# Optimization experiments

Hardware: AMD Instinct MI355X
Metric: run time of the kernel (lower is better)

The kernel has to match this reference:

```python
import jax, jax.numpy as jnp
import numpy as np

D_MODEL = 1024
N_HEADS = 16
D_K = D_MODEL // N_HEADS
D_FF = 4096
B, S = 4, 2048
EPS = 1e-5


def setup_inputs() -> dict:
    key = jax.random.key(0)
    ks = jax.random.split(key, 16)
    s = 0.02
    inp = {
        'x': jax.random.normal(ks[0], (B, S, D_MODEL), dtype=jnp.float32),
        'Wq': jax.random.normal(ks[1], (D_MODEL, D_MODEL), dtype=jnp.float32) * s,
        'bq': jnp.zeros((D_MODEL,), jnp.float32),
        'Wk': jax.random.normal(ks[2], (D_MODEL, D_MODEL), dtype=jnp.float32) * s,
        'bk': jnp.zeros((D_MODEL,), jnp.float32),
        'Wv': jax.random.normal(ks[3], (D_MODEL, D_MODEL), dtype=jnp.float32) * s,
        'bv': jnp.zeros((D_MODEL,), jnp.float32),
        'Wo': jax.random.normal(ks[4], (D_MODEL, D_MODEL), dtype=jnp.float32) * s,
        'bo': jnp.zeros((D_MODEL,), jnp.float32),
        'W1': jax.random.normal(ks[5], (D_MODEL, D_FF), dtype=jnp.float32) * s,
        'b1': jnp.zeros((D_FF,), jnp.float32),
        'W2': jax.random.normal(ks[6], (D_FF, D_MODEL), dtype=jnp.float32) * s,
        'b2': jnp.zeros((D_MODEL,), jnp.float32),
        'g1': jnp.ones((D_MODEL,), jnp.float32),
        'be1': jnp.zeros((D_MODEL,), jnp.float32),
        'g2': jnp.ones((D_MODEL,), jnp.float32),
        'be2': jnp.zeros((D_MODEL,), jnp.float32),
    }
    return inp


def _layernorm(x, g, b):
    mu = jnp.mean(x, axis=-1, keepdims=True)
    var = jnp.var(x, axis=-1, keepdims=True)
    return (x - mu) * jax.lax.rsqrt(var + EPS) * g + b


def reference(x, Wq, bq, Wk, bk, Wv, bv, Wo, bo, W1, b1, W2, b2, g1, be1, g2, be2):
    # Multi-head self-attention (mask=None, dropout in eval -> identity)
    q = (x @ Wq + bq).reshape(B, S, N_HEADS, D_K).transpose(0, 2, 1, 3)  # [B,H,S,Dk]
    k = (x @ Wk + bk).reshape(B, S, N_HEADS, D_K).transpose(0, 2, 1, 3)
    v = (x @ Wv + bv).reshape(B, S, N_HEADS, D_K).transpose(0, 2, 1, 3)
    scores = jnp.einsum('bhqd,bhkd->bhqk', q, k) / jnp.sqrt(jnp.float32(D_K))
    attn = jax.nn.softmax(scores, axis=-1)
    out = jnp.einsum('bhqk,bhkd->bhqd', attn, v)          # [B,H,S,Dk]
    out = out.transpose(0, 2, 1, 3).reshape(B, S, D_MODEL)
    att_out = out @ Wo + bo
    x2 = _layernorm(x + att_out, g1, be1)
    ff = jax.nn.relu(x2 @ W1 + b1) @ W2 + b2
    return _layernorm(x2 + ff, g2, be2)
```

## Files before the change

kernel.cpp:

```cpp
#include <hip/hip_runtime.h>
#include <hip/hip_bf16.h>

typedef __attribute__((ext_vector_type(8)))  __bf16 bf16x8;
typedef __attribute__((ext_vector_type(4)))  float  f32x4;
typedef __attribute__((ext_vector_type(16))) float  f32x16;

static __device__ __forceinline__ unsigned short f2bf(float x) {
    unsigned int u = __float_as_uint(x);
    unsigned int r = (u + 0x7FFFu + ((u >> 16) & 1u)) >> 16;
    return (unsigned short)r;
}

static __device__ __forceinline__ float fast_exp2(float x) {
    float r;
    asm volatile("v_exp_f32 %0, %1\n\ts_nop 1" : "=v"(r) : "v"(x));
    return r;
}
static __device__ __forceinline__ unsigned int cvt_pk_bf16(float a, float b) {
    unsigned int r;
    asm("v_cvt_pk_bf16_f32 %0, %1, %2" : "=v"(r) : "v"(a), "v"(b));
    return r;
}

static __device__ __forceinline__ void gload_lds16(const ushort* g, ushort* l) {
    __builtin_amdgcn_global_load_lds((const __attribute__((address_space(1))) void*)g,
                                     (__attribute__((address_space(3))) void*)l, 16, 0, 0);
}

static __device__ __forceinline__ int xcd_swz(int id, int nwg) {
    return (id & 7) * (nwg >> 3) + (id >> 3);
}

__global__ __launch_bounds__(256) void cast_bf16_kernel(const float* __restrict__ in,
                                                        ushort* __restrict__ out, int n4) {
    int i = blockIdx.x * 256 + threadIdx.x;
    if (i < n4) {
        float4 v = reinterpret_cast<const float4*>(in)[i];
        ushort4 o;
        o.x = f2bf(v.x); o.y = f2bf(v.y); o.z = f2bf(v.z); o.w = f2bf(v.w);
        reinterpret_cast<ushort4*>(out)[i] = o;
    }
}

__global__ __launch_bounds__(256) void transpose_cast_kernel(const float* __restrict__ in,
                                                             ushort* __restrict__ out,
                                                             int K, int N) {
    __shared__ float tile[32][33];
    const int tx = threadIdx.x;
    const int ty = threadIdx.y;
    const int n0 = blockIdx.x * 32;
    const int k0 = blockIdx.y * 32;
    for (int i = ty; i < 32; i += 8)
        tile[i][tx] = in[(size_t)(k0 + i) * N + n0 + tx];
    __syncthreads();
    for (int i = ty; i < 32; i += 8)
        out[(size_t)(n0 + i) * K + k0 + tx] = f2bf(tile[tx][i]);
}

template<int RELU, int OUTBF>
__global__ __launch_bounds__(256) void gemm_bt(const ushort* __restrict__ A,
                                               const ushort* __restrict__ Bt,
                                               const float* __restrict__ bias,
                                               void* __restrict__ Cp,
                                               int M, int N, int K) {
    __shared__ ushort As[128 * 32];
    __shared__ ushort Bs[128 * 32];
    const int tid  = threadIdx.x;
    const int lane = tid & 63;
    const int w    = tid >> 6;
    const int wr   = w >> 1, wc = w & 1;
    const int nwg = gridDim.x * gridDim.y;
    int wid = xcd_swz(blockIdx.y * gridDim.x + blockIdx.x, nwg);
    const int bx = wid % gridDim.x;
    const int by = wid / gridDim.x;
    const int m0 = by * 128;
    const int n0 = bx * 128;
    const int lr = lane & 15;
    const int lk = (lane >> 4) * 8;

    const int r0 = w * 32 + (lane >> 2);
    const int c8 = (lane & 3) * 8;
    const ushort* gA0 = A  + (size_t)(m0 + r0)      * K + c8;
    const ushort* gA1 = A  + (size_t)(m0 + r0 + 16) * K + c8;
    const ushort* gB0 = Bt + (size_t)(n0 + r0)      * K + c8;
    const ushort* gB1 = Bt + (size_t)(n0 + r0 + 16) * K + c8;
    ushort* lA0 = &As[w * 1024];
    ushort* lA1 = &As[w * 1024 + 512];
    ushort* lB0 = &Bs[w * 1024];
    ushort* lB1 = &Bs[w * 1024 + 512];

    f32x4 acc[4][4];
    const f32x4 z = {0.f, 0.f, 0.f, 0.f};
    for (int i = 0; i < 4; i++) for (int j = 0; j < 4; j++) acc[i][j] = z;

    for (int k0 = 0; k0 < K; k0 += 32) {
        __syncthreads();
        gload_lds16(gA0 + k0, lA0);
        gload_lds16(gA1 + k0, lA1);
        gload_lds16(gB0 + k0, lB0);
        gload_lds16(gB1 + k0, lB1);
        __syncthreads();

        bf16x8 af[4], bfr[4];
        for (int i = 0; i < 4; i++)
            af[i] = *reinterpret_cast<const bf16x8*>(&As[(wr * 64 + i * 16 + lr) * 32 + lk]);
        for (int j = 0; j < 4; j++)
            bfr[j] = *reinterpret_cast<const bf16x8*>(&Bs[(wc * 64 + j * 16 + lr) * 32 + lk]);
        for (int i = 0; i < 4; i++)
            for (int j = 0; j < 4; j++)
                acc[i][j] = __builtin_amdgcn_mfma_f32_16x16x32_bf16(af[i], bfr[j], acc[i][j], 0, 0, 0);
    }

    const int rbase = (lane >> 4) * 4;
    for (int i = 0; i < 4; i++) {
        for (int j = 0; j < 4; j++) {
            const int col = n0 + wc * 64 + j * 16 + lr;
            const float bv = bias[col];
            for (int r = 0; r < 4; r++) {
                const int row = m0 + wr * 64 + i * 16 + rbase + r;
                float v = acc[i][j][r] + bv;
                if (RELU) v = v > 0.f ? v : 0.f;
                if (OUTBF) ((ushort*)Cp)[(size_t)row * N + col] = f2bf(v);
                else       ((float*)Cp)[(size_t)row * N + col] = v;
            }
        }
    }
}

__global__ __launch_bounds__(256) void gemm_qkv(const ushort* __restrict__ A,
                                                const ushort* __restrict__ Bt,
                                                const float* __restrict__ bq,
                                                const float* __restrict__ bk,
                                                const float* __restrict__ bv,
                                                ushort* __restrict__ Cp) {
    const int K = 1024, N = 3072;
    __shared__ ushort As[128 * 32];
    __shared__ ushort Bs[128 * 32];
    const int tid  = threadIdx.x;
    const int lane = tid & 63;
    const int w    = tid >> 6;
    const int wr   = w >> 1, wc = w & 1;
    const int nwg = gridDim.x * gridDim.y;
    int wid = xcd_swz(blockIdx.y * gridDim.x + blockIdx.x, nwg);
    const int bx = wid % gridDim.x;
    const int by = wid / gridDim.x;
    const int m0 = by * 128;
    const int n0 = bx * 128;
    const int lr = lane & 15;
    const int lk = (lane >> 4) * 8;

    const int r0 = w * 32 + (lane >> 2);
    const int c8 = (lane & 3) * 8;
    const ushort* gA0 = A  + (size_t)(m0 + r0)      * K + c8;
    const ushort* gA1 = A  + (size_t)(m0 + r0 + 16) * K + c8;
    const ushort* gB0 = Bt + (size_t)(n0 + r0)      * K + c8;
    const ushort* gB1 = Bt + (size_t)(n0 + r0 + 16) * K + c8;
    ushort* lA0 = &As[w * 1024];
    ushort* lA1 = &As[w * 1024 + 512];
    ushort* lB0 = &Bs[w * 1024];
    ushort* lB1 = &Bs[w * 1024 + 512];

    f32x4 acc[4][4];
    const f32x4 z = {0.f, 0.f, 0.f, 0.f};
    for (int i = 0; i < 4; i++) for (int j = 0; j < 4; j++) acc[i][j] = z;

    for (int k0 = 0; k0 < K; k0 += 32) {
        __syncthreads();
        gload_lds16(gA0 + k0, lA0);
        gload_lds16(gA1 + k0, lA1);
        gload_lds16(gB0 + k0, lB0);
        gload_lds16(gB1 + k0, lB1);
        __syncthreads();

        bf16x8 af[4], bfr[4];
        for (int i = 0; i < 4; i++)
            af[i] = *reinterpret_cast<const bf16x8*>(&As[(wr * 64 + i * 16 + lr) * 32 + lk]);
        for (int j = 0; j < 4; j++)
            bfr[j] = *reinterpret_cast<const bf16x8*>(&Bs[(wc * 64 + j * 16 + lr) * 32 + lk]);
        for (int i = 0; i < 4; i++)
            for (int j = 0; j < 4; j++)
                acc[i][j] = __builtin_amdgcn_mfma_f32_16x16x32_bf16(af[i], bfr[j], acc[i][j], 0, 0, 0);
    }

    const float* bias = (n0 < 1024) ? bq : (n0 < 2048 ? bk : bv);
    const float qscale = (n0 < 1024) ? 0.18033688f : 1.0f;
    const int nb = n0 & 1023;
    const int rbase = (lane >> 4) * 4;
    for (int i = 0; i < 4; i++) {
        for (int j = 0; j < 4; j++) {
            const int cloc = wc * 64 + j * 16 + lr;
            const float bv_ = bias[nb + cloc];
            for (int r = 0; r < 4; r++) {
                const int row = m0 + wr * 64 + i * 16 + rbase + r;
                Cp[(size_t)row * 3072 + n0 + cloc] = f2bf((acc[i][j][r] + bv_) * qscale);
            }
        }
    }
}

#define ASWZ(row, col) ((row) * 64 + ((col) ^ ((((row) ^ ((row) >> 3)) & 7) << 3)))

__global__ __launch_bounds__(256, 3) void attn_kernel(const ushort* __restrict__ QKV,
                                                      ushort* __restrict__ O) {
    __shared__ ushort Ks[2][4096];
    __shared__ ushort Vt[2][4096];
    __shared__ ushort Ps[4][2048];
    const int tid  = threadIdx.x;
    const int lane = tid & 63;
    const int w    = tid >> 6;
    const int l31  = lane & 31;
    const int hi   = lane >> 5;

    int blk = xcd_swz(blockIdx.x, gridDim.x);
    const int qb = blk & 15;
    const int h  = (blk >> 4) & 15;
    const int b  = blk >> 8;
    const int s0 = qb * 128 + w * 32;
    const size_t rowb   = (size_t)b * 2048;
    const size_t base_q = rowb * 3072 + (size_t)h * 64;
    const size_t base_k = base_q + 1024;
    const size_t base_v = base_q + 2048;
    const size_t base_o = rowb * 1024 + (size_t)h * 64;

    bf16x8 qf[4];
#pragma unroll
    for (int ks = 0; ks < 4; ks++)
        qf[ks] = *reinterpret_cast<const bf16x8*>(
            &QKV[base_q + (size_t)(s0 + l31) * 3072 + ks * 16 + 8 * hi]);

    int off8[2][4];
#pragma unroll
    for (int sub = 0; sub < 2; sub++)
#pragma unroll
        for (int ks = 0; ks < 4; ks++)
            off8[sub][ks] = ASWZ(sub * 32 + l31, ks * 16 + 8 * hi);
    int psoff[2][4][2];
#pragma unroll
    for (int ts = 0; ts < 2; ts++)
#pragma unroll
        for (int q4 = 0; q4 < 4; q4++)
#pragma unroll
            for (int e = 0; e < 2; e++)
                psoff[ts][q4][e] = ASWZ(l31, ts * 32 + 8 * q4 + 4 * hi + 2 * e);

    const int tS  = tid >> 3;
    const int ccS = tid & 7;
    int vwoff[2][8];
#pragma unroll
    for (int i = 0; i < 2; i++)
#pragma unroll
        for (int jj = 0; jj < 8; jj++)
            vwoff[i][jj] = ASWZ(ccS * 8 + jj, tS + i * 32);
    const int t1  = tS + 32;
    const int sz0 = (tS ^ (tS >> 3)) & 7;
    const int sz1 = (t1 ^ (t1 >> 3)) & 7;
    const ushort* pK0 = QKV + base_k + (size_t)tS * 3072 + (ccS ^ sz0) * 8;
    const ushort* pK1 = QKV + base_k + (size_t)t1 * 3072 + (ccS ^ sz1) * 8;
    const ushort* pV0 = QKV + base_v + (size_t)tS * 3072 + ccS * 8;
    const ushort* pV1 = QKV + base_v + (size_t)t1 * 3072 + ccS * 8;
    const size_t step = (size_t)64 * 3072;
    ushort* psw = Ps[w];

    gload_lds16(pK0, &Ks[0][w * 512]);
    gload_lds16(pK1, &Ks[0][2048 + w * 512]);
    {
        int4 v0 = *reinterpret_cast<const int4*>(pV0);
        int4 v1 = *reinterpret_cast<const int4*>(pV1);
        const ushort* vs0 = reinterpret_cast<const ushort*>(&v0);
        const ushort* vs1 = reinterpret_cast<const ushort*>(&v1);
#pragma unroll
        for (int jj = 0; jj < 8; jj++) Vt[0][vwoff[0][jj]] = vs0[jj];
#pragma unroll
        for (int jj = 0; jj < 8; jj++) Vt[0][vwoff[1][jj]] = vs1[jj];
    }
    pK0 += step; pK1 += step; pV0 += step; pV1 += step;
    __syncthreads();

    f32x16 oacc0 = {0.f}, oacc1 = {0.f};
    for (int i = 0; i < 16; i++) { oacc0[i] = 0.f; oacc1[i] = 0.f; }
    float lacc = 0.f;
    int cur = 0;

    for (int it = 0; it < 32; ++it) {
        int4 nv0, nv1;
        if (it < 31) {
            gload_lds16(pK0, &Ks[cur ^ 1][w * 512]);
            gload_lds16(pK1, &Ks[cur ^ 1][2048 + w * 512]);
            nv0 = *reinterpret_cast<const int4*>(pV0);
            nv1 = *reinterpret_cast<const int4*>(pV1);
            pK0 += step; pK1 += step; pV0 += step; pV1 += step;
        }

        f32x16 sa0 = {0.f}, sa1 = {0.f};
        for (int i = 0; i < 16; i++) { sa0[i] = 0.f; sa1[i] = 0.f; }
        __builtin_amdgcn_s_setprio(1);
#pragma unroll
        for (int ks = 0; ks < 4; ks++) {
            bf16x8 k0 = *reinterpret_cast<const bf16x8*>(&Ks[cur][off8[0][ks]]);
            sa0 = __builtin_amdgcn_mfma_f32_32x32x16_bf16(k0, qf[ks], sa0, 0, 0, 0);
        }
#pragma unroll
        for (int ks = 0; ks < 4; ks++) {
            bf16x8 k1 = *reinterpret_cast<const bf16x8*>(&Ks[cur][off8[1][ks]]);
            sa1 = __builtin_amdgcn_mfma_f32_32x32x16_bf16(k1, qf[ks], sa1, 0, 0, 0);
        }
        __builtin_amdgcn_s_setprio(0);

#pragma unroll
        for (int q4 = 0; q4 < 4; q4++)
#pragma unroll
            for (int e = 0; e < 2; e++) {
                float plo = fast_exp2(sa0[4 * q4 + 2 * e]);
                float phi = fast_exp2(sa0[4 * q4 + 2 * e + 1]);
                lacc += plo + phi;
                *reinterpret_cast<unsigned int*>(&psw[psoff[0][q4][e]]) = cvt_pk_bf16(plo, phi);
            }
#pragma unroll
        for (int q4 = 0; q4 < 4; q4++)
#pragma unroll
            for (int e = 0; e < 2; e++) {
                float plo = fast_exp2(sa1[4 * q4 + 2 * e]);
                float phi = fast_exp2(sa1[4 * q4 + 2 * e + 1]);
                lacc += plo + phi;
                *reinterpret_cast<unsigned int*>(&psw[psoff[1][q4][e]]) = cvt_pk_bf16(plo, phi);
            }

        __builtin_amdgcn_s_setprio(1);
#pragma unroll
        for (int ks = 0; ks < 4; ks++) {
            bf16x8 pa = *reinterpret_cast<const bf16x8*>(&psw[off8[0][ks]]);
            bf16x8 v0 = *reinterpret_cast<const bf16x8*>(&Vt[cur][off8[0][ks]]);
            oacc0 = __builtin_amdgcn_mfma_f32_32x32x16_bf16(pa, v0, oacc0, 0, 0, 0);
            bf16x8 v1 = *reinterpret_cast<const bf16x8*>(&Vt[cur][off8[1][ks]]);
            oacc1 = __builtin_amdgcn_mfma_f32_32x32x16_bf16(pa, v1, oacc1, 0, 0, 0);
        }
        __builtin_amdgcn_s_setprio(0);

        if (it < 31) {
            const ushort* vs0 = reinterpret_cast<const ushort*>(&nv0);
            const ushort* vs1 = reinterpret_cast<const ushort*>(&nv1);
#pragma unroll
            for (int jj = 0; jj < 8; jj++) Vt[cur ^ 1][vwoff[0][jj]] = vs0[jj];
#pragma unroll
            for (int jj = 0; jj < 8; jj++) Vt[cur ^ 1][vwoff[1][jj]] = vs1[jj];
        }
        __syncthreads();
        cur ^= 1;
    }

    const float ltot = lacc + __shfl_xor(lacc, 32);
    const float inv  = 1.f / ltot;

#pragma unroll
    for (int r = 0; r < 16; r++) {
        const int qloc = (r & 3) + 8 * (r >> 2) + 4 * hi;
        const float invq = __shfl(inv, qloc);
        const size_t rowoff = base_o + (size_t)(s0 + qloc) * 1024 + l31;
        O[rowoff]      = f2bf(oacc0[r] * invq);
        O[rowoff + 32] = f2bf(oacc1[r] * invq);
    }
}

__global__ __launch_bounds__(256) void ln_res_kernel(const float* __restrict__ x,
                                                     const float* __restrict__ y,
                                                     const float* __restrict__ g,
                                                     const float* __restrict__ be,
                                                     float* __restrict__ outf,
                                                     ushort* __restrict__ outb) {
    const int row = blockIdx.x;
    const int tid = threadIdx.x;
    const float4 xv = reinterpret_cast<const float4*>(x + (size_t)row * 1024)[tid];
    const float4 yv = reinterpret_cast<const float4*>(y + (size_t)row * 1024)[tid];
    float v[4] = {xv.x + yv.x, xv.y + yv.y, xv.z + yv.z, xv.w + yv.w};
    float s  = v[0] + v[1] + v[2] + v[3];
    float s2 = v[0]*v[0] + v[1]*v[1] + v[2]*v[2] + v[3]*v[3];
    for (int off = 32; off; off >>= 1) { s += __shfl_down(s, off); s2 += __shfl_down(s2, off); }
    __shared__ float red[8];
    const int w = tid >> 6, lane = tid & 63;
    if (lane == 0) { red[w] = s; red[4 + w] = s2; }
    __syncthreads();
    if (tid == 0) {
        const float ts  = red[0] + red[1] + red[2] + red[3];
        const float ts2 = red[4] + red[5] + red[6] + red[7];
        const float mu  = ts * (1.f / 1024.f);
        const float var = ts2 * (1.f / 1024.f) - mu * mu;
        red[0] = mu;
        red[1] = rsqrtf(var + 1e-5f);
    }
    __syncthreads();
    const float mu = red[0], rs = red[1];
    float4 of;
    ushort4 ob;
    const float4 gv = reinterpret_cast<const float4*>(g)[tid];
    const float4 bv = reinterpret_cast<const float4*>(be)[tid];
    of.x = (v[0] - mu) * rs * gv.x + bv.x;
    of.y = (v[1] - mu) * rs * gv.y + bv.y;
    of.z = (v[2] - mu) * rs * gv.z + bv.z;
    of.w = (v[3] - mu) * rs * gv.w + bv.w;
    reinterpret_cast<float4*>(outf + (size_t)row * 1024)[tid] = of;
    if (outb) {
        ob.x = f2bf(of.x); ob.y = f2bf(of.y); ob.z = f2bf(of.z); ob.w = f2bf(of.w);
        reinterpret_cast<ushort4*>(outb + (size_t)row * 1024)[tid] = ob;
    }
}

extern "C" void kernel_launch(void* const* d_in, const int* in_sizes, int n_in,
                              void* d_out, int out_size, void* d_ws, size_t ws_size,
                              hipStream_t stream) {
    const float* x  = (const float*)d_in[0];
    const float* Wq = (const float*)d_in[1];  const float* bq = (const float*)d_in[2];
    const float* Wk = (const float*)d_in[3];  const float* bk = (const float*)d_in[4];
    const float* Wv = (const float*)d_in[5];  const float* bv = (const float*)d_in[6];
    const float* Wo = (const float*)d_in[7];  const float* bo = (const float*)d_in[8];
    const float* W1 = (const float*)d_in[9];  const float* b1 = (const float*)d_in[10];
    const float* W2 = (const float*)d_in[11]; const float* b2 = (const float*)d_in[12];
    const float* g1 = (const float*)d_in[13]; const float* be1 = (const float*)d_in[14];
    const float* g2 = (const float*)d_in[15]; const float* be2 = (const float*)d_in[16];

    char* ws = (char*)d_ws;
    const size_t MBy = (size_t)1 << 20;
    ushort* xb    = (ushort*)(ws + 0 * MBy);
    ushort* wqkvT = (ushort*)(ws + 16 * MBy);
    ushort* woT   = (ushort*)(ws + 22 * MBy);
    ushort* w1T   = (ushort*)(ws + 24 * MBy);
    ushort* w2T   = (ushort*)(ws + 32 * MBy);
    ushort* QKVb  = (ushort*)(ws + 40 * MBy);
    ushort* AOb   = (ushort*)(ws + 88 * MBy);
    ushort* h1    = (ushort*)(ws + 40 * MBy);
    float*  y1    = (float*)(ws + 104 * MBy);
    float*  y2    = (float*)(ws + 104 * MBy);
    float*  x2f   = (float*)(ws + 136 * MBy);
    ushort* x2b   = (ushort*)(ws + 168 * MBy);
    (void)ws_size; (void)n_in; (void)in_sizes; (void)out_size;

    const int M = 8192;

    cast_bf16_kernel<<<(M * 1024 / 4 + 255) / 256, 256, 0, stream>>>(x, xb, M * 1024 / 4);
    dim3 tb(32, 8);
    transpose_cast_kernel<<<dim3(32, 32),  tb, 0, stream>>>(Wq, wqkvT,               1024, 1024);
    transpose_cast_kernel<<<dim3(32, 32),  tb, 0, stream>>>(Wk, wqkvT + 1024 * 1024, 1024, 1024);
    transpose_cast_kernel<<<dim3(32, 32),  tb, 0, stream>>>(Wv, wqkvT + 2048 * 1024, 1024, 1024);
    transpose_cast_kernel<<<dim3(32, 32),  tb, 0, stream>>>(Wo, woT, 1024, 1024);
    transpose_cast_kernel<<<dim3(128, 32), tb, 0, stream>>>(W1, w1T, 1024, 4096);
    transpose_cast_kernel<<<dim3(32, 128), tb, 0, stream>>>(W2, w2T, 4096, 1024);

    gemm_qkv<<<dim3(24, 64), 256, 0, stream>>>(xb, wqkvT, bq, bk, bv, QKVb);

    attn_kernel<<<1024, 256, 0, stream>>>(QKVb, AOb);

    gemm_bt<0, 0><<<dim3(8, 64), 256, 0, stream>>>(AOb, woT, bo, y1, M, 1024, 1024);

    ln_res_kernel<<<M, 256, 0, stream>>>(x, y1, g1, be1, x2f, x2b);

    gemm_bt<1, 1><<<dim3(32, 64), 256, 0, stream>>>(x2b, w1T, b1, h1, M, 4096, 1024);
    gemm_bt<0, 0><<<dim3(8, 64), 256, 0, stream>>>(h1, w2T, b2, y2, M, 1024, 4096);

    ln_res_kernel<<<M, 256, 0, stream>>>(x2f, y2, g2, be2, (float*)d_out, nullptr);
}
```

Before: 469.5 us.

## Keep P in registers via permlane swap; store intermediates as bf16

In the attention kernel the softmax probabilities were written to a per-wave LDS buffer and read back as the MFMA A operand. They are now packed in registers, and v_permlane32_swap rearranges them into operand layout, which removes that LDS traffic and frees its shared memory. Separately, the Wo and W2 GEMM outputs, and the residual x2 fed into the second layernorm, are stored as bf16 instead of fp32. This cuts global memory traffic in the GEMM epilogues and layernorm kernels. The cost is lower precision on the residual and pre-norm sums.

```diff
diff --git a/kernel.cpp b/kernel.cpp
--- a/kernel.cpp
+++ b/kernel.cpp
@@ -9,6 +9,9 @@
     unsigned int u = __float_as_uint(x);
     unsigned int r = (u + 0x7FFFu + ((u >> 16) & 1u)) >> 16;
     return (unsigned short)r;
+}
+static __device__ __forceinline__ float bf2f(unsigned short u) {
+    return __uint_as_float(((unsigned int)u) << 16);
 }
 
 static __device__ __forceinline__ float fast_exp2(float x) {
@@ -133,7 +136,7 @@
                                                 const float* __restrict__ bk,
                                                 const float* __restrict__ bv,
                                                 ushort* __restrict__ Cp) {
-    const int K = 1024, N = 3072;
+    const int K = 1024;
     __shared__ ushort As[128 * 32];
     __shared__ ushort Bs[128 * 32];
     const int tid  = threadIdx.x;
@@ -204,7 +207,6 @@
                                                       ushort* __restrict__ O) {
     __shared__ ushort Ks[2][4096];
     __shared__ ushort Vt[2][4096];
-    __shared__ ushort Ps[4][2048];
     const int tid  = threadIdx.x;
     const int lane = tid & 63;
     const int w    = tid >> 6;
@@ -234,14 +236,6 @@
 #pragma unroll
         for (int ks = 0; ks < 4; ks++)
             off8[sub][ks] = ASWZ(sub * 32 + l31, ks * 16 + 8 * hi);
-    int psoff[2][4][2];
-#pragma unroll
-    for (int ts = 0; ts < 2; ts++)
-#pragma unroll
-        for (int q4 = 0; q4 < 4; q4++)
-#pragma unroll
-            for (int e = 0; e < 2; e++)
-                psoff[ts][q4][e] = ASWZ(l31, ts * 32 + 8 * q4 + 4 * hi + 2 * e);
 
     const int tS  = tid >> 3;
     const int ccS = tid & 7;
@@ -259,7 +253,6 @@
     const ushort* pV0 = QKV + base_v + (size_t)tS * 3072 + ccS * 8;
     const ushort* pV1 = QKV + base_v + (size_t)t1 * 3072 + ccS * 8;
     const size_t step = (size_t)64 * 3072;
-    ushort* psw = Ps[w];
 
     gload_lds16(pK0, &Ks[0][w * 512]);
     gload_lds16(pK1, &Ks[0][2048 + w * 512]);
@@ -276,7 +269,7 @@
     pK0 += step; pK1 += step; pV0 += step; pV1 += step;
     __syncthreads();
 
-    f32x16 oacc0 = {0.f}, oacc1 = {0.f};
+    f32x16 oacc0, oacc1;
     for (int i = 0; i < 16; i++) { oacc0[i] = 0.f; oacc1[i] = 0.f; }
     float lacc = 0.f;
     int cur = 0;
@@ -291,7 +284,7 @@
             pK0 += step; pK1 += step; pV0 += step; pV1 += step;
         }
 
-        f32x16 sa0 = {0.f}, sa1 = {0.f};
+        f32x16 sa0, sa1;
         for (int i = 0; i < 16; i++) { sa0[i] = 0.f; sa1[i] = 0.f; }
         __builtin_amdgcn_s_setprio(1);
 #pragma unroll
@@ -306,33 +299,37 @@
         }
         __builtin_amdgcn_s_setprio(0);
 
-#pragma unroll
-        for (int q4 = 0; q4 < 4; q4++)
-#pragma unroll
-            for (int e = 0; e < 2; e++) {
-                float plo = fast_exp2(sa0[4 * q4 + 2 * e]);
-                float phi = fast_exp2(sa0[4 * q4 + 2 * e + 1]);
-                lacc += plo + phi;
-                *reinterpret_cast<unsigned int*>(&psw[psoff[0][q4][e]]) = cvt_pk_bf16(plo, phi);
-            }
-#pragma unroll
-        for (int q4 = 0; q4 < 4; q4++)
-#pragma unroll
-            for (int e = 0; e < 2; e++) {
-                float plo = fast_exp2(sa1[4 * q4 + 2 * e]);
-                float phi = fast_exp2(sa1[4 * q4 + 2 * e + 1]);
-                lacc += plo + phi;
-                *reinterpret_cast<unsigned int*>(&psw[psoff[1][q4][e]]) = cvt_pk_bf16(plo, phi);
-            }
+        unsigned pk0[8], pk1[8];
+#pragma unroll
+        for (int i = 0; i < 8; i++) {
+            float plo = fast_exp2(sa0[2 * i]);
+            float phi = fast_exp2(sa0[2 * i + 1]);
+            lacc += plo + phi;
+            pk0[i] = cvt_pk_bf16(plo, phi);
+        }
+#pragma unroll
+        for (int i = 0; i < 8; i++) {
+            float plo = fast_exp2(sa1[2 * i]);
+            float phi = fast_exp2(sa1[2 * i + 1]);
+            lacc += plo + phi;
+            pk1[i] = cvt_pk_bf16(plo, phi);
+        }
 
         __builtin_amdgcn_s_setprio(1);
 #pragma unroll
         for (int ks = 0; ks < 4; ks++) {
-            bf16x8 pa = *reinterpret_cast<const bf16x8*>(&psw[off8[0][ks]]);
+            const int bi = 4 * (ks & 1);
+            unsigned a, bb, c, d;
+            if (ks < 2) { a = pk0[bi]; bb = pk0[bi + 1]; c = pk0[bi + 2]; d = pk0[bi + 3]; }
+            else        { a = pk1[bi]; bb = pk1[bi + 1]; c = pk1[bi + 2]; d = pk1[bi + 3]; }
+            asm("v_permlane32_swap_b32 %0, %1" : "+v"(a), "+v"(c));
+            asm("v_permlane32_swap_b32 %0, %1" : "+v"(bb), "+v"(d));
+            union { unsigned u[4]; bf16x8 v; } fr;
+            fr.u[0] = a; fr.u[1] = bb; fr.u[2] = c; fr.u[3] = d;
             bf16x8 v0 = *reinterpret_cast<const bf16x8*>(&Vt[cur][off8[0][ks]]);
-            oacc0 = __builtin_amdgcn_mfma_f32_32x32x16_bf16(pa, v0, oacc0, 0, 0, 0);
+            oacc0 = __builtin_amdgcn_mfma_f32_32x32x16_bf16(fr.v, v0, oacc0, 0, 0, 0);
             bf16x8 v1 = *reinterpret_cast<const bf16x8*>(&Vt[cur][off8[1][ks]]);
-            oacc1 = __builtin_amdgcn_mfma_f32_32x32x16_bf16(pa, v1, oacc1, 0, 0, 0);
+            oacc1 = __builtin_amdgcn_mfma_f32_32x32x16_bf16(fr.v, v1, oacc1, 0, 0, 0);
         }
         __builtin_amdgcn_s_setprio(0);
 
@@ -361,17 +358,16 @@
     }
 }
 
-__global__ __launch_bounds__(256) void ln_res_kernel(const float* __restrict__ x,
-                                                     const float* __restrict__ y,
-                                                     const float* __restrict__ g,
-                                                     const float* __restrict__ be,
-                                                     float* __restrict__ outf,
-                                                     ushort* __restrict__ outb) {
+__global__ __launch_bounds__(256) void ln_res_fb(const float* __restrict__ x,
+                                                 const ushort* __restrict__ y,
+                                                 const float* __restrict__ g,
+                                                 const float* __restrict__ be,
+                                                 ushort* __restrict__ outb) {
     const int row = blockIdx.x;
     const int tid = threadIdx.x;
     const float4 xv = reinterpret_cast<const float4*>(x + (size_t)row * 1024)[tid];
-    const float4 yv = reinterpret_cast<const float4*>(y + (size_t)row * 1024)[tid];
-    float v[4] = {xv.x + yv.x, xv.y + yv.y, xv.z + yv.z, xv.w + yv.w};
+    const ushort4 yv = reinterpret_cast<const ushort4*>(y + (size_t)row * 1024)[tid];
+    float v[4] = {xv.x + bf2f(yv.x), xv.y + bf2f(yv.y), xv.z + bf2f(yv.z), xv.w + bf2f(yv.w)};
     float s  = v[0] + v[1] + v[2] + v[3];
     float s2 = v[0]*v[0] + v[1]*v[1] + v[2]*v[2] + v[3]*v[3];
     for (int off = 32; off; off >>= 1) { s += __shfl_down(s, off); s2 += __shfl_down(s2, off); }
@@ -389,19 +385,52 @@
     }
     __syncthreads();
     const float mu = red[0], rs = red[1];
-    float4 of;
-    ushort4 ob;
     const float4 gv = reinterpret_cast<const float4*>(g)[tid];
     const float4 bv = reinterpret_cast<const float4*>(be)[tid];
+    ushort4 ob;
+    ob.x = f2bf((v[0] - mu) * rs * gv.x + bv.x);
+    ob.y = f2bf((v[1] - mu) * rs * gv.y + bv.y);
+    ob.z = f2bf((v[2] - mu) * rs * gv.z + bv.z);
+    ob.w = f2bf((v[3] - mu) * rs * gv.w + bv.w);
+    reinterpret_cast<ushort4*>(outb + (size_t)row * 1024)[tid] = ob;
+}
+
+__global__ __launch_bounds__(256) void ln_res_bb(const ushort* __restrict__ x,
+                                                 const ushort* __restrict__ y,
+                                                 const float* __restrict__ g,
+                                                 const float* __restrict__ be,
+                                                 float* __restrict__ outf) {
+    const int row = blockIdx.x;
+    const int tid = threadIdx.x;
+    const ushort4 xv = reinterpret_cast<const ushort4*>(x + (size_t)row * 1024)[tid];
+    const ushort4 yv = reinterpret_cast<const ushort4*>(y + (size_t)row * 1024)[tid];
+    float v[4] = {bf2f(xv.x) + bf2f(yv.x), bf2f(xv.y) + bf2f(yv.y),
+                  bf2f(xv.z) + bf2f(yv.z), bf2f(xv.w) + bf2f(yv.w)};
+    float s  = v[0] + v[1] + v[2] + v[3];
+    float s2 = v[0]*v[0] + v[1]*v[1] + v[2]*v[2] + v[3]*v[3];
+    for (int off = 32; off; off >>= 1) { s += __shfl_down(s, off); s2 += __shfl_down(s2, off); }
+    __shared__ float red[8];
+    const int w = tid >> 6, lane = tid & 63;
+    if (lane == 0) { red[w] = s; red[4 + w] = s2; }
+    __syncthreads();
+    if (tid == 0) {
+        const float ts  = red[0] + red[1] + red[2] + red[3];
+        const float ts2 = red[4] + red[5] + red[6] + red[7];
+        const float mu  = ts * (1.f / 1024.f);
+        const float var = ts2 * (1.f / 1024.f) - mu * mu;
+        red[0] = mu;
+        red[1] = rsqrtf(var + 1e-5f);
+    }
+    __syncthreads();
+    const float mu = red[0], rs = red[1];
+    const float4 gv = reinterpret_cast<const float4*>(g)[tid];
+    const float4 bv = reinterpret_cast<const float4*>(be)[tid];
+    float4 of;
     of.x = (v[0] - mu) * rs * gv.x + bv.x;
     of.y = (v[1] - mu) * rs * gv.y + bv.y;
     of.z = (v[2] - mu) * rs * gv.z + bv.z;
     of.w = (v[3] - mu) * rs * gv.w + bv.w;
     reinterpret_cast<float4*>(outf + (size_t)row * 1024)[tid] = of;
-    if (outb) {
-        ob.x = f2bf(of.x); ob.y = f2bf(of.y); ob.z = f2bf(of.z); ob.w = f2bf(of.w);
-        reinterpret_cast<ushort4*>(outb + (size_t)row * 1024)[tid] = ob;
-    }
 }
 
 extern "C" void kernel_launch(void* const* d_in, const int* in_sizes, int n_in,
@@ -427,10 +456,9 @@
     ushort* QKVb  = (ushort*)(ws + 40 * MBy);
     ushort* AOb   = (ushort*)(ws + 88 * MBy);
     ushort* h1    = (ushort*)(ws + 40 * MBy);
-    float*  y1    = (float*)(ws + 104 * MBy);
-    float*  y2    = (float*)(ws + 104 * MBy);
-    float*  x2f   = (float*)(ws + 136 * MBy);
-    ushort* x2b   = (ushort*)(ws + 168 * MBy);
+    ushort* y1b   = (ushort*)(ws + 104 * MBy);
+    ushort* y2b   = (ushort*)(ws + 104 * MBy);
+    ushort* x2b   = (ushort*)(ws + 120 * MBy);
     (void)ws_size; (void)n_in; (void)in_sizes; (void)out_size;
 
     const int M = 8192;
@@ -448,12 +476,12 @@
 
     attn_kernel<<<1024, 256, 0, stream>>>(QKVb, AOb);
 
-    gemm_bt<0, 0><<<dim3(8, 64), 256, 0, stream>>>(AOb, woT, bo, y1, M, 1024, 1024);
-
-    ln_res_kernel<<<M, 256, 0, stream>>>(x, y1, g1, be1, x2f, x2b);
+    gemm_bt<0, 1><<<dim3(8, 64), 256, 0, stream>>>(AOb, woT, bo, y1b, M, 1024, 1024);
+
+    ln_res_fb<<<M, 256, 0, stream>>>(x, y1b, g1, be1, x2b);
 
     gemm_bt<1, 1><<<dim3(32, 64), 256, 0, stream>>>(x2b, w1T, b1, h1, M, 4096, 1024);
-    gemm_bt<0, 0><<<dim3(8, 64), 256, 0, stream>>>(h1, w2T, b2, y2, M, 1024, 4096);
-
-    ln_res_kernel<<<M, 256, 0, stream>>>(x2f, y2, g2, be2, (float*)d_out, nullptr);
-}
+    gemm_bt<0, 1><<<dim3(8, 64), 256, 0, stream>>>(h1, w2T, b2, y2b, M, 1024, 4096);
+
+    ln_res_bb<<<M, 256, 0, stream>>>(x2b, y2b, g2, be2, (float*)d_out);
+}
```

After: 450.8 us. -4.0%, faster.
